# Optimization experiments

Hardware: AMD Instinct MI355X
Metric: run time of the kernel (lower is better)

Reference implementation:

```python
import jax, jax.numpy as jnp
import numpy as np

N, D, E, H, K = 16384, 256, 8, 512, 2


def setup_inputs() -> dict:
    key = jax.random.key(0)
    ks = jax.random.split(key, 5)
    inputs = jax.random.normal(ks[0], (N, D), dtype=jnp.float32)
    Wg = jax.random.normal(ks[1], (D, E), dtype=jnp.float32) * 0.05
    w1 = jax.random.normal(ks[2], (E, D, H), dtype=jnp.float32) * 0.05
    b1 = jnp.zeros((E, H), dtype=jnp.float32)
    w2 = jax.random.normal(ks[3], (E, H, D), dtype=jnp.float32) * 0.05
    b2 = jnp.zeros((E, D), dtype=jnp.float32)
    return {"inputs": inputs, "Wg": Wg, "w1": w1, "b1": b1, "w2": w2, "b2": b2}


def reference(inputs, Wg, w1, b1, w2, b2):
    # gate + top-k routing (softmax over the selected logits only, as in the torch code)
    gate_logits = inputs @ Wg                       # [N, E]
    topw, topi = jax.lax.top_k(gate_logits, K)      # [N, K]
    topw = jax.nn.softmax(topw.astype(jnp.float32), axis=1).astype(inputs.dtype)
    # combine weights scattered back into a dense [N, E] matrix (dispatch/combine)
    combine = jnp.zeros((N, E), dtype=inputs.dtype)
    combine = combine.at[jnp.arange(N)[:, None], topi].add(topw)  # [N, E]
    # expert MLP (Linear -> GELU(exact) -> Linear), computed per expert and
    # combined with the sparse routing weights (pool='sum')
    h = jax.nn.gelu(jnp.einsum('nd,edh->neh', inputs, w1) + b1[None], approximate=False)  # [N,E,H]
    y = jnp.einsum('neh,ehd->ned', h, w2) + b2[None]                                      # [N,E,D]
    return jnp.einsum('ne,ned->nd', combine, y)                                           # [N,D]
```

## Files before the change

kernel.cpp:

```cpp
#include <hip/hip_runtime.h>

#define NTOK 16384
#define DIM 256
#define NEXP 8
#define HID 512
#define CAP 5120
#define CSTRIDE 16

typedef unsigned short ushort_t;
typedef short bf16x8 __attribute__((ext_vector_type(8)));
typedef float f32x4 __attribute__((ext_vector_type(4)));

static __device__ __forceinline__ ushort_t f2bf(float f) {
    unsigned int u = __float_as_uint(f);
    unsigned int r = (u + 0x7FFFu + ((u >> 16) & 1u)) >> 16;
    return (ushort_t)r;
}
static __device__ __forceinline__ float bf2f(ushort_t u) {
    unsigned int x = ((unsigned int)u) << 16;
    return __uint_as_float(x);
}
static __device__ __forceinline__ float gelu_fast(float v) {
    float v3 = v * v * v;
    float u = -1.5957691216f * v - 0.0713548163f * v3;
    return v / (1.0f + __expf(u));
}

__global__ void k_transpose(const float* __restrict__ w1, const float* __restrict__ w2,
                            ushort_t* __restrict__ w1t, ushort_t* __restrict__ w2t,
                            int* __restrict__ counts) {
    __shared__ ushort_t tile[64][72];
    if (blockIdx.x == 0 && threadIdx.x < NEXP * CSTRIDE) counts[threadIdx.x] = 0;
    int b = blockIdx.x;
    const float* src; ushort_t* dst; int R, C, e, t;
    if (b < 256) { e = b >> 5; t = b & 31; src = w1; dst = w1t + e * DIM * HID; R = DIM; C = HID; }
    else { b -= 256; e = b >> 5; t = b & 31; src = w2; dst = w2t + e * DIM * HID; R = HID; C = DIM; }
    size_t ebase = (size_t)e * DIM * HID;
    int tilesC = C >> 6;
    int rt = t / tilesC, ct = t % tilesC;
    for (int i = 0; i < 16; i++) {
        int flat = i * 256 + threadIdx.x;
        int lr = flat >> 6, lc = flat & 63;
        tile[lr][lc] = f2bf(src[ebase + (size_t)(rt * 64 + lr) * C + ct * 64 + lc]);
    }
    __syncthreads();
    for (int i = 0; i < 16; i++) {
        int flat = i * 256 + threadIdx.x;
        int lr = flat >> 6, lc = flat & 63;
        dst[(ct * 64 + lr) * R + rt * 64 + lc] = tile[lc][lr];
    }
}

__global__ void k_router(const float* __restrict__ X, const float* __restrict__ Wg,
                         int* counts, int* tok_list, int* inv_idx, float* inv_w,
                         ushort_t* __restrict__ Xb) {
    __shared__ float xs[64][257];
    __shared__ float lg[64][8];
    __shared__ int te0[64], te1[64], lo0[64], lo1[64];
    __shared__ float tw0[64], tw1[64];
    __shared__ int lcnt[NEXP], gbase[NEXP];
    int tid = threadIdx.x;
    int tok0 = blockIdx.x * 64;
    if (tid < NEXP) lcnt[tid] = 0;
    for (int i = 0; i < 8; i++) {
        int flat = i * 256 + tid;
        int r = flat >> 5, c8 = (flat & 31) << 3;
        const float* row = X + (size_t)(tok0 + r) * DIM + c8;
        float4 a = *(const float4*)row;
        float4 b = *(const float4*)(row + 4);
        xs[r][c8 + 0] = a.x; xs[r][c8 + 1] = a.y; xs[r][c8 + 2] = a.z; xs[r][c8 + 3] = a.w;
        xs[r][c8 + 4] = b.x; xs[r][c8 + 5] = b.y; xs[r][c8 + 6] = b.z; xs[r][c8 + 7] = b.w;
    }
    __syncthreads();
    for (int i = 0; i < 8; i++) {
        int flat = i * 256 + tid;
        int r = flat >> 5, c8 = (flat & 31) << 3;
        ushort_t pk[8];
#pragma unroll
        for (int j = 0; j < 8; j++) pk[j] = f2bf(xs[r][c8 + j]);
        *(int4*)(Xb + (size_t)(tok0 + r) * DIM + c8) = *(const int4*)pk;
    }
    int tl = tid & 63, pair = tid >> 6;
    float l0 = 0.f, l1 = 0.f;
    for (int d = 0; d < DIM; d++) {
        float x = xs[tl][d];
        l0 += x * Wg[d * NEXP + 2 * pair];
        l1 += x * Wg[d * NEXP + 2 * pair + 1];
    }
    lg[tl][2 * pair] = l0; lg[tl][2 * pair + 1] = l1;
    __syncthreads();
    if (tid < 64) {
        float best = -1e30f; int bi = 0;
#pragma unroll
        for (int e = 0; e < NEXP; e++) { float v = lg[tid][e]; if (v > best) { best = v; bi = e; } }
        float best2 = -1e30f; int bi2 = 0;
#pragma unroll
        for (int e = 0; e < NEXP; e++) { if (e == bi) continue; float v = lg[tid][e]; if (v > best2) { best2 = v; bi2 = e; } }
        float ed = __expf(best2 - best);
        te0[tid] = bi; te1[tid] = bi2;
        tw0[tid] = 1.0f / (1.0f + ed);
        tw1[tid] = ed / (1.0f + ed);
        lo0[tid] = atomicAdd(&lcnt[bi], 1);
        lo1[tid] = atomicAdd(&lcnt[bi2], 1);
    }
    __syncthreads();
    if (tid < NEXP) gbase[tid] = atomicAdd(&counts[tid * CSTRIDE], lcnt[tid]);
    __syncthreads();
    if (tid < 64) {
        int token = tok0 + tid;
        int e0 = te0[tid], e1 = te1[tid];
        int p0 = gbase[e0] + lo0[tid]; if (p0 >= CAP) p0 = CAP - 1;
        int p1 = gbase[e1] + lo1[tid]; if (p1 >= CAP) p1 = CAP - 1;
        tok_list[e0 * CAP + p0] = token;
        tok_list[e1 * CAP + p1] = token;
        inv_idx[token * 2]     = (e0 << 16) | p0;  inv_w[token * 2]     = tw0[tid];
        inv_idx[token * 2 + 1] = (e1 << 16) | p1;  inv_w[token * 2 + 1] = tw1[tid];
    }
}

__launch_bounds__(512, 4)
__global__ void k_mlp1(const ushort_t* __restrict__ Xb, const ushort_t* __restrict__ w1t,
                       const float* __restrict__ b1,
                       const int* __restrict__ counts, const int* __restrict__ tok_list,
                       ushort_t* __restrict__ hb) {
    __shared__ ushort_t B1[128 * 264];
    int b = blockIdx.x;
    int e = b / (40 * 4);
    int rem = b % (40 * 4);
    int tile = rem >> 2, hq = rem & 3;
    int count = counts[e * CSTRIDE];
    if (count > CAP) count = CAP;
    int t0 = tile * 128;
    if (t0 >= count) return;

    int tid = threadIdx.x;
    int w = tid >> 6, l = tid & 63, ln = l & 15, q = l >> 4;

    const ushort_t* w1te = w1t + (size_t)e * DIM * HID + (size_t)hq * 128 * DIM;
#pragma unroll
    for (int i = 0; i < 8; i++) {
        int flat = i * 512 + tid;
        int hr = flat >> 5, c8 = (flat & 31) << 3;
        *(int4*)(B1 + hr * 264 + c8) = *(const int4*)(w1te + hr * DIM + c8);
    }
    int arow = t0 + 16 * w + ln;
    int ci = (arow < count) ? arow : (count - 1);
    int atok = tok_list[e * CAP + ci];
    const ushort_t* xrow = Xb + (size_t)atok * DIM;
    bf16x8 xf[8];
#pragma unroll
    for (int ks = 0; ks < 8; ks++)
        xf[ks] = *(const bf16x8*)(xrow + ks * 32 + q * 8);
    __syncthreads();

    f32x4 zf = {0.f, 0.f, 0.f, 0.f};
    f32x4 acc[8];
#pragma unroll
    for (int i = 0; i < 8; i++) acc[i] = zf;
#pragma unroll
    for (int ks = 0; ks < 8; ks++) {
        bf16x8 xk = xf[ks];
#pragma unroll
        for (int cf = 0; cf < 8; cf++) {
            bf16x8 wfr = *(const bf16x8*)(B1 + (cf * 16 + ln) * 264 + ks * 32 + q * 8);
            acc[cf] = __builtin_amdgcn_mfma_f32_16x16x32_bf16(wfr, xk, acc[cf], 0, 0, 0);
        }
    }
    size_t hrowbase = ((size_t)e * CAP + t0 + 16 * w + ln) * HID + hq * 128;
#pragma unroll
    for (int cf = 0; cf < 8; cf++) {
        float4 bv = *(const float4*)(b1 + e * HID + hq * 128 + cf * 16 + q * 4);
        ushort4 pk;
        pk.x = f2bf(gelu_fast(acc[cf][0] + bv.x));
        pk.y = f2bf(gelu_fast(acc[cf][1] + bv.y));
        pk.z = f2bf(gelu_fast(acc[cf][2] + bv.z));
        pk.w = f2bf(gelu_fast(acc[cf][3] + bv.w));
        *(ushort4*)(hb + hrowbase + cf * 16 + q * 4) = pk;
    }
}

__launch_bounds__(256, 2)
__global__ void k_mlp2(const ushort_t* __restrict__ hb, const ushort_t* __restrict__ w2t,
                       const float* __restrict__ b2,
                       const int* __restrict__ counts, ushort_t* __restrict__ yb) {
    __shared__ ushort_t B2[64 * 520];
    int b = blockIdx.x;
    int e = b / (80 * 4);
    int rem = b % (80 * 4);
    int tile = rem >> 2, dq = rem & 3;
    int count = counts[e * CSTRIDE];
    if (count > CAP) count = CAP;
    int t0 = tile * 64;
    if (t0 >= count) return;

    int tid = threadIdx.x;
    int w = tid >> 6, l = tid & 63, ln = l & 15, q = l >> 4;

    const ushort_t* w2te = w2t + (size_t)e * DIM * HID + (size_t)dq * 64 * HID;
#pragma unroll
    for (int i = 0; i < 16; i++) {
        int flat = i * 256 + tid;
        int dr = flat >> 6, c8 = (flat & 63) << 3;
        *(int4*)(B2 + dr * 520 + c8) = *(const int4*)(w2te + dr * HID + c8);
    }
    int arow = t0 + 16 * w + ln;
    int ci = (arow < count) ? arow : (count - 1);
    const ushort_t* hrow = hb + ((size_t)e * CAP + ci) * HID;
    bf16x8 af[16];
#pragma unroll
    for (int ks = 0; ks < 16; ks++)
        af[ks] = *(const bf16x8*)(hrow + ks * 32 + q * 8);
    __syncthreads();

    f32x4 zf = {0.f, 0.f, 0.f, 0.f};
    f32x4 acc[4];
#pragma unroll
    for (int i = 0; i < 4; i++) acc[i] = zf;
#pragma unroll
    for (int ks = 0; ks < 16; ks++) {
        bf16x8 hk = af[ks];
#pragma unroll
        for (int cf = 0; cf < 4; cf++) {
            bf16x8 wfr = *(const bf16x8*)(B2 + (cf * 16 + ln) * 520 + ks * 32 + q * 8);
            acc[cf] = __builtin_amdgcn_mfma_f32_16x16x32_bf16(wfr, hk, acc[cf], 0, 0, 0);
        }
    }
    size_t yrowbase = ((size_t)e * CAP + t0 + 16 * w + ln) * DIM + dq * 64;
#pragma unroll
    for (int cf = 0; cf < 4; cf++) {
        float4 bv = *(const float4*)(b2 + e * DIM + dq * 64 + cf * 16 + q * 4);
        ushort4 pk;
        pk.x = f2bf(acc[cf][0] + bv.x);
        pk.y = f2bf(acc[cf][1] + bv.y);
        pk.z = f2bf(acc[cf][2] + bv.z);
        pk.w = f2bf(acc[cf][3] + bv.w);
        *(ushort4*)(yb + yrowbase + cf * 16 + q * 4) = pk;
    }
}

__global__ void k_combine(const ushort_t* __restrict__ yb, const int* __restrict__ inv_idx,
                          const float* __restrict__ inv_w, float* __restrict__ out) {
    int tid = threadIdx.x;
    int n = blockIdx.x * 8 + (tid >> 5);
    int l32 = tid & 31, c8 = l32 << 3;
    int i0 = inv_idx[2 * n], i1 = inv_idx[2 * n + 1];
    float w0 = inv_w[2 * n], w1 = inv_w[2 * n + 1];
    size_t r0 = (size_t)(i0 >> 16) * CAP + (i0 & 0xFFFF);
    size_t r1 = (size_t)(i1 >> 16) * CAP + (i1 & 0xFFFF);
    int4 v0 = *(const int4*)(yb + r0 * DIM + c8);
    int4 v1 = *(const int4*)(yb + r1 * DIM + c8);
    ushort_t* p0 = (ushort_t*)&v0;
    ushort_t* p1 = (ushort_t*)&v1;
    float4 oa, ob;
    oa.x = w0 * bf2f(p0[0]) + w1 * bf2f(p1[0]);
    oa.y = w0 * bf2f(p0[1]) + w1 * bf2f(p1[1]);
    oa.z = w0 * bf2f(p0[2]) + w1 * bf2f(p1[2]);
    oa.w = w0 * bf2f(p0[3]) + w1 * bf2f(p1[3]);
    ob.x = w0 * bf2f(p0[4]) + w1 * bf2f(p1[4]);
    ob.y = w0 * bf2f(p0[5]) + w1 * bf2f(p1[5]);
    ob.z = w0 * bf2f(p0[6]) + w1 * bf2f(p1[6]);
    ob.w = w0 * bf2f(p0[7]) + w1 * bf2f(p1[7]);
    float4* op = (float4*)(out + (size_t)n * DIM + c8);
    op[0] = oa; op[1] = ob;
}

extern "C" void kernel_launch(void* const* d_in, const int* in_sizes, int n_in,
                              void* d_out, int out_size, void* d_ws, size_t ws_size,
                              hipStream_t stream) {
    const float* X  = (const float*)d_in[0];
    const float* Wg = (const float*)d_in[1];
    const float* w1 = (const float*)d_in[2];
    const float* b1 = (const float*)d_in[3];
    const float* w2 = (const float*)d_in[4];
    const float* b2 = (const float*)d_in[5];

    char* ws = (char*)d_ws;
    size_t off = 0;
    int* counts = (int*)(ws + off);        off = 1024;
    int* tok_list = (int*)(ws + off);      off += (size_t)NEXP * CAP * 4;
    int* inv_idx = (int*)(ws + off);       off += (size_t)NTOK * 2 * 4;
    float* inv_w = (float*)(ws + off);     off += (size_t)NTOK * 2 * 4;
    ushort_t* w1t = (ushort_t*)(ws + off); off += (size_t)NEXP * DIM * HID * 2;
    ushort_t* w2t = (ushort_t*)(ws + off); off += (size_t)NEXP * DIM * HID * 2;
    ushort_t* Xb = (ushort_t*)(ws + off);  off += (size_t)NTOK * DIM * 2;
    ushort_t* hb = (ushort_t*)(ws + off);  off += (size_t)NEXP * CAP * HID * 2;
    ushort_t* yb = (ushort_t*)(ws + off);  off += (size_t)NEXP * CAP * DIM * 2;

    k_transpose<<<512, 256, 0, stream>>>(w1, w2, w1t, w2t, counts);
    k_router<<<256, 256, 0, stream>>>(X, Wg, counts, tok_list, inv_idx, inv_w, Xb);
    k_mlp1<<<NEXP * 40 * 4, 512, 0, stream>>>(Xb, w1t, b1, counts, tok_list, hb);
    k_mlp2<<<NEXP * 80 * 4, 256, 0, stream>>>(hb, w2t, b2, counts, yb);
    k_combine<<<2048, 256, 0, stream>>>(yb, inv_idx, inv_w, (float*)d_out);
}
```

Before: 164.2 us.

## Switch expert MLP GEMMs to 32x32x16 MFMA with larger tiles and faster GELU

Both expert MLP kernels move from 16x16x32 to 32x32x16 bf16 MFMA. Each wave now owns 32 token rows, so k_mlp1 runs 256-thread blocks and k_mlp2 uses 128-row tiles with half as many blocks, each staging its weight slice once. The larger MFMA shape raises data reuse per LDS fragment load, and k_mlp2 loads its activations in two K halves to limit register pressure. The GELU approximation now uses exp2 and rcp intrinsics, and out-of-range rows skip their stores. The trade-off is fewer blocks per expert, which may lower occupancy and parallelism.

```diff
diff --git a/kernel.cpp b/kernel.cpp
--- a/kernel.cpp
+++ b/kernel.cpp
@@ -10,6 +10,7 @@
 typedef unsigned short ushort_t;
 typedef short bf16x8 __attribute__((ext_vector_type(8)));
 typedef float f32x4 __attribute__((ext_vector_type(4)));
+typedef float f32x16 __attribute__((ext_vector_type(16)));
 
 static __device__ __forceinline__ ushort_t f2bf(float f) {
     unsigned int u = __float_as_uint(f);
@@ -21,9 +22,10 @@
     return __uint_as_float(x);
 }
 static __device__ __forceinline__ float gelu_fast(float v) {
-    float v3 = v * v * v;
-    float u = -1.5957691216f * v - 0.0713548163f * v3;
-    return v / (1.0f + __expf(u));
+    float v2 = v * v;
+    float u = v * __builtin_fmaf(v2, -0.1029407079f, -2.3022090196f);
+    float e = __builtin_amdgcn_exp2f(u);
+    return v * __builtin_amdgcn_rcpf(1.0f + e);
 }
 
 __global__ void k_transpose(const float* __restrict__ w1, const float* __restrict__ w2,
@@ -118,15 +120,15 @@
     }
 }
 
-__launch_bounds__(512, 4)
+__launch_bounds__(256, 2)
 __global__ void k_mlp1(const ushort_t* __restrict__ Xb, const ushort_t* __restrict__ w1t,
                        const float* __restrict__ b1,
                        const int* __restrict__ counts, const int* __restrict__ tok_list,
                        ushort_t* __restrict__ hb) {
     __shared__ ushort_t B1[128 * 264];
     int b = blockIdx.x;
-    int e = b / (40 * 4);
-    int rem = b % (40 * 4);
+    int e = b / 160;
+    int rem = b % 160;
     int tile = rem >> 2, hq = rem & 3;
     int count = counts[e * CSTRIDE];
     if (count > CAP) count = CAP;
@@ -134,48 +136,53 @@
     if (t0 >= count) return;
 
     int tid = threadIdx.x;
-    int w = tid >> 6, l = tid & 63, ln = l & 15, q = l >> 4;
+    int w = tid >> 6, l = tid & 63, m = l & 31, hi = l >> 5;
 
     const ushort_t* w1te = w1t + (size_t)e * DIM * HID + (size_t)hq * 128 * DIM;
 #pragma unroll
-    for (int i = 0; i < 8; i++) {
-        int flat = i * 512 + tid;
+    for (int i = 0; i < 16; i++) {
+        int flat = i * 256 + tid;
         int hr = flat >> 5, c8 = (flat & 31) << 3;
         *(int4*)(B1 + hr * 264 + c8) = *(const int4*)(w1te + hr * DIM + c8);
     }
-    int arow = t0 + 16 * w + ln;
+    int arow = t0 + 32 * w + m;
     int ci = (arow < count) ? arow : (count - 1);
     int atok = tok_list[e * CAP + ci];
     const ushort_t* xrow = Xb + (size_t)atok * DIM;
-    bf16x8 xf[8];
-#pragma unroll
-    for (int ks = 0; ks < 8; ks++)
-        xf[ks] = *(const bf16x8*)(xrow + ks * 32 + q * 8);
-    __syncthreads();
-
-    f32x4 zf = {0.f, 0.f, 0.f, 0.f};
-    f32x4 acc[8];
-#pragma unroll
-    for (int i = 0; i < 8; i++) acc[i] = zf;
-#pragma unroll
-    for (int ks = 0; ks < 8; ks++) {
+    bf16x8 xf[16];
+#pragma unroll
+    for (int ks = 0; ks < 16; ks++)
+        xf[ks] = *(const bf16x8*)(xrow + ks * 16 + hi * 8);
+    __syncthreads();
+
+    f32x16 acc[4];
+#pragma unroll
+    for (int i = 0; i < 4; i++) acc[i] = (f32x16)(0.0f);
+#pragma unroll
+    for (int ks = 0; ks < 16; ks++) {
         bf16x8 xk = xf[ks];
 #pragma unroll
-        for (int cf = 0; cf < 8; cf++) {
-            bf16x8 wfr = *(const bf16x8*)(B1 + (cf * 16 + ln) * 264 + ks * 32 + q * 8);
-            acc[cf] = __builtin_amdgcn_mfma_f32_16x16x32_bf16(wfr, xk, acc[cf], 0, 0, 0);
+        for (int cf = 0; cf < 4; cf++) {
+            bf16x8 wfr = *(const bf16x8*)(B1 + (cf * 32 + m) * 264 + ks * 16 + hi * 8);
+            acc[cf] = __builtin_amdgcn_mfma_f32_32x32x16_bf16(wfr, xk, acc[cf], 0, 0, 0);
         }
     }
-    size_t hrowbase = ((size_t)e * CAP + t0 + 16 * w + ln) * HID + hq * 128;
-#pragma unroll
-    for (int cf = 0; cf < 8; cf++) {
-        float4 bv = *(const float4*)(b1 + e * HID + hq * 128 + cf * 16 + q * 4);
-        ushort4 pk;
-        pk.x = f2bf(gelu_fast(acc[cf][0] + bv.x));
-        pk.y = f2bf(gelu_fast(acc[cf][1] + bv.y));
-        pk.z = f2bf(gelu_fast(acc[cf][2] + bv.z));
-        pk.w = f2bf(gelu_fast(acc[cf][3] + bv.w));
-        *(ushort4*)(hb + hrowbase + cf * 16 + q * 4) = pk;
+    if (arow < count) {
+        ushort_t* hrow = hb + ((size_t)e * CAP + arow) * HID + hq * 128;
+#pragma unroll
+        for (int cf = 0; cf < 4; cf++) {
+#pragma unroll
+            for (int rg = 0; rg < 4; rg++) {
+                int hoff = cf * 32 + 8 * rg + 4 * hi;
+                float4 bv = *(const float4*)(b1 + e * HID + hq * 128 + hoff);
+                ushort4 pk;
+                pk.x = f2bf(gelu_fast(acc[cf][rg * 4 + 0] + bv.x));
+                pk.y = f2bf(gelu_fast(acc[cf][rg * 4 + 1] + bv.y));
+                pk.z = f2bf(gelu_fast(acc[cf][rg * 4 + 2] + bv.z));
+                pk.w = f2bf(gelu_fast(acc[cf][rg * 4 + 3] + bv.w));
+                *(ushort4*)(hrow + hoff) = pk;
+            }
+        }
     }
 }
 
@@ -185,16 +192,16 @@
                        const int* __restrict__ counts, ushort_t* __restrict__ yb) {
     __shared__ ushort_t B2[64 * 520];
     int b = blockIdx.x;
-    int e = b / (80 * 4);
-    int rem = b % (80 * 4);
+    int e = b / 160;
+    int rem = b % 160;
     int tile = rem >> 2, dq = rem & 3;
     int count = counts[e * CSTRIDE];
     if (count > CAP) count = CAP;
-    int t0 = tile * 64;
+    int t0 = tile * 128;
     if (t0 >= count) return;
 
     int tid = threadIdx.x;
-    int w = tid >> 6, l = tid & 63, ln = l & 15, q = l >> 4;
+    int w = tid >> 6, l = tid & 63, m = l & 31, hi = l >> 5;
 
     const ushort_t* w2te = w2t + (size_t)e * DIM * HID + (size_t)dq * 64 * HID;
 #pragma unroll
@@ -203,38 +210,45 @@
         int dr = flat >> 6, c8 = (flat & 63) << 3;
         *(int4*)(B2 + dr * 520 + c8) = *(const int4*)(w2te + dr * HID + c8);
     }
-    int arow = t0 + 16 * w + ln;
+    int arow = t0 + 32 * w + m;
     int ci = (arow < count) ? arow : (count - 1);
     const ushort_t* hrow = hb + ((size_t)e * CAP + ci) * HID;
-    bf16x8 af[16];
-#pragma unroll
-    for (int ks = 0; ks < 16; ks++)
-        af[ks] = *(const bf16x8*)(hrow + ks * 32 + q * 8);
-    __syncthreads();
-
-    f32x4 zf = {0.f, 0.f, 0.f, 0.f};
-    f32x4 acc[4];
-#pragma unroll
-    for (int i = 0; i < 4; i++) acc[i] = zf;
-#pragma unroll
-    for (int ks = 0; ks < 16; ks++) {
-        bf16x8 hk = af[ks];
-#pragma unroll
-        for (int cf = 0; cf < 4; cf++) {
-            bf16x8 wfr = *(const bf16x8*)(B2 + (cf * 16 + ln) * 520 + ks * 32 + q * 8);
-            acc[cf] = __builtin_amdgcn_mfma_f32_16x16x32_bf16(wfr, hk, acc[cf], 0, 0, 0);
+    __syncthreads();
+
+    f32x16 acc[2];
+    acc[0] = (f32x16)(0.0f); acc[1] = (f32x16)(0.0f);
+#pragma unroll
+    for (int kh = 0; kh < 2; kh++) {
+        bf16x8 hf[16];
+#pragma unroll
+        for (int ks = 0; ks < 16; ks++)
+            hf[ks] = *(const bf16x8*)(hrow + kh * 256 + ks * 16 + hi * 8);
+#pragma unroll
+        for (int ks = 0; ks < 16; ks++) {
+            bf16x8 hk = hf[ks];
+#pragma unroll
+            for (int cf = 0; cf < 2; cf++) {
+                bf16x8 wfr = *(const bf16x8*)(B2 + (cf * 32 + m) * 520 + kh * 256 + ks * 16 + hi * 8);
+                acc[cf] = __builtin_amdgcn_mfma_f32_32x32x16_bf16(wfr, hk, acc[cf], 0, 0, 0);
+            }
         }
     }
-    size_t yrowbase = ((size_t)e * CAP + t0 + 16 * w + ln) * DIM + dq * 64;
-#pragma unroll
-    for (int cf = 0; cf < 4; cf++) {
-        float4 bv = *(const float4*)(b2 + e * DIM + dq * 64 + cf * 16 + q * 4);
-        ushort4 pk;
-        pk.x = f2bf(acc[cf][0] + bv.x);
-        pk.y = f2bf(acc[cf][1] + bv.y);
-        pk.z = f2bf(acc[cf][2] + bv.z);
-        pk.w = f2bf(acc[cf][3] + bv.w);
-        *(ushort4*)(yb + yrowbase + cf * 16 + q * 4) = pk;
+    if (arow < count) {
+        ushort_t* yrow = yb + ((size_t)e * CAP + arow) * DIM + dq * 64;
+#pragma unroll
+        for (int cf = 0; cf < 2; cf++) {
+#pragma unroll
+            for (int rg = 0; rg < 4; rg++) {
+                int doff = cf * 32 + 8 * rg + 4 * hi;
+                float4 bv = *(const float4*)(b2 + e * DIM + dq * 64 + doff);
+                ushort4 pk;
+                pk.x = f2bf(acc[cf][rg * 4 + 0] + bv.x);
+                pk.y = f2bf(acc[cf][rg * 4 + 1] + bv.y);
+                pk.z = f2bf(acc[cf][rg * 4 + 2] + bv.z);
+                pk.w = f2bf(acc[cf][rg * 4 + 3] + bv.w);
+                *(ushort4*)(yrow + doff) = pk;
+            }
+        }
     }
 }
 
@@ -288,7 +302,7 @@
 
     k_transpose<<<512, 256, 0, stream>>>(w1, w2, w1t, w2t, counts);
     k_router<<<256, 256, 0, stream>>>(X, Wg, counts, tok_list, inv_idx, inv_w, Xb);
-    k_mlp1<<<NEXP * 40 * 4, 512, 0, stream>>>(Xb, w1t, b1, counts, tok_list, hb);
-    k_mlp2<<<NEXP * 80 * 4, 256, 0, stream>>>(hb, w2t, b2, counts, yb);
+    k_mlp1<<<NEXP * 40 * 4, 256, 0, stream>>>(Xb, w1t, b1, counts, tok_list, hb);
+    k_mlp2<<<NEXP * 40 * 4, 256, 0, stream>>>(hb, w2t, b2, counts, yb);
     k_combine<<<2048, 256, 0, stream>>>(yb, inv_idx, inv_w, (float*)d_out);
 }
```

New measurement: 169.6 us. 1.03x slower.
